# Kernel tuning notes

Measured on AMD Instinct MI355X. Metric: run time of the kernel, lower is better.

Reference implementation:

```python
import jax, jax.numpy as jnp
import numpy as np

# positions 0,1 = input tensor dims; positions 2,3 = output tensor dims (single entity type)

def _set_partitions(elems):
    if not elems:
        yield []
        return
    first, rest = elems[0], elems[1:]
    for p in _set_partitions(rest):
        for i in range(len(p)):
            yield p[:i] + [p[i] + [first]] + p[i + 1:]
    # note: generator above already covers merging; add singleton case

def _all_set_partitions(elems):
    if not elems:
        return [[]]
    first, rest = elems[0], elems[1:]
    out = []
    for p in _all_set_partitions(rest):
        for i in range(len(p)):
            out.append(p[:i] + [p[i] + [first]] + p[i + 1:])
        out.append([[first]] + p)
    return out

PARTITIONS = _all_set_partitions([0, 1, 2, 3])  # Bell(4) = 15 equivariant partitions


def _apply_partition(X, part, eye, ones):
    """Dense equivalent of diag -> pool -> broadcast -> undiag -> reindex for one partition.
    X: [b, c, n, n]. Returns [b, c, n, n]."""
    pos2blk = {p: bi for bi, blk in enumerate(part) for p in blk}
    blk_letter = {bi: 'defg'[bi] for bi in range(len(part))}
    # step 1: diag (repeated letters) + pool (letters dropped from output)
    in_sub = 'bc' + blk_letter[pos2blk[0]] + blk_letter[pos2blk[1]]
    keep = [bi for bi, blk in enumerate(part)
            if any(p < 2 for p in blk) and any(p >= 2 for p in blk)]
    z_sub = 'bc' + ''.join(blk_letter[bi] for bi in keep)
    Z = jnp.einsum(f'{in_sub}->{z_sub}', X)
    # step 2: broadcast + diag-embed into output positions via eye/ones factors
    out_letter = {2: 'p', 3: 'q'}
    operands, subs = [Z], [z_sub]
    for bi, blk in enumerate(part):
        outpos = [p for p in blk if p >= 2]
        if not outpos:
            continue
        if any(p < 2 for p in blk):  # block tied to a surviving input dim
            for p in outpos:
                operands.append(eye)
                subs.append(blk_letter[bi] + out_letter[p])
        else:  # pure broadcast block
            first = outpos[0]
            operands.append(ones)
            subs.append(out_letter[first])
            for p in outpos[1:]:
                operands.append(eye)
                subs.append(out_letter[first] + out_letter[p])
    return jnp.einsum(','.join(subs) + '->bcpq', *operands)


def setup_inputs() -> dict:
    key = jax.random.key(0)
    k1, k2 = jax.random.split(key)
    B, C_IN, C_OUT, N = 4, 96, 96, 256
    stdv = 0.1 / np.sqrt(C_IN)
    X_in = jax.random.normal(k1, (B, C_IN, N, N), dtype=jnp.float32)
    Y_in = jnp.zeros((B, C_IN, N, N), dtype=jnp.float32)  # only provides output shape
    weights = jax.random.uniform(k2, (15, C_IN, C_OUT), minval=-stdv, maxval=stdv, dtype=jnp.float32)
    bias = jnp.ones((1,), dtype=jnp.float32)
    return {'X_in': X_in, 'Y_in': Y_in, 'weights': weights, 'bias': bias}


def reference(X_in, Y_in, weights, bias):
    n = X_in.shape[-1]
    eye = jnp.eye(n, dtype=X_in.dtype)
    ones = jnp.ones((n,), dtype=X_in.dtype)
    Y = None
    for i, part in enumerate(PARTITIONS):
        Yp = _apply_partition(X_in, part, eye, ones)          # [b, c_in, n, n]
        Yp = jnp.einsum('bcpq,co->bopq', Yp, weights[i])       # channel linear
        Y = Yp if Y is None else Y + Yp
    return Y + bias[0]
```

## Files before the change

### kernel.cpp

```cpp
#include <hip/hip_runtime.h>
#include <hip/hip_bf16.h>

#define NN 256
#define CIN 96
#define COUT 96
#define BB 4
#define NBC (BB * CIN)
#define SEG (NBC * NN)

typedef __attribute__((ext_vector_type(8))) short short8;
typedef __attribute__((ext_vector_type(4))) float f32x4;

__device__ __forceinline__ float waveReduceSum(float v) {
    #pragma unroll
    for (int m = 32; m >= 1; m >>= 1) v += __shfl_xor(v, m, 64);
    return v;
}

__device__ __forceinline__ unsigned int packbf2(float lo, float hi) {
    __hip_bfloat162 h = __float22bfloat162_rn(make_float2(lo, hi));
    unsigned int u;
    __builtin_memcpy(&u, &h, 4);
    return u;
}

__device__ __forceinline__ short8 u4_to_s8(uint4 u) {
    short8 r;
    __builtin_memcpy(&r, &u, 16);
    return r;
}

__device__ __forceinline__ void lds_barrier() {
    __builtin_amdgcn_sched_barrier(0);
    asm volatile("s_waitcnt lgkmcnt(0)" ::: "memory");
    __builtin_amdgcn_s_barrier();
    __builtin_amdgcn_sched_barrier(0);
}

__global__ __launch_bounds__(256) void k_aux(const float* __restrict__ X,
                                             float* __restrict__ rows,
                                             float* __restrict__ diag,
                                             float* __restrict__ colsP,
                                             float* __restrict__ TSp) {
    const int blk = blockIdx.x;
    const int ch = blk & 3, bc = blk >> 2;
    const float* Xp = X + (size_t)bc * (NN * NN) + (size_t)ch * 64 * NN;
    const int tid = threadIdx.x;
    const int w = tid >> 6, lane = tid & 63;

    __shared__ float colPart[4][NN];
    __shared__ float sred[4];

    float4 csum = make_float4(0.f, 0.f, 0.f, 0.f);
    #pragma unroll
    for (int b2 = 0; b2 < 2; ++b2) {
        float4 v[8];
        #pragma unroll
        for (int j = 0; j < 8; ++j) {
            const int r = w * 16 + b2 * 8 + j;
            v[j] = *(const float4*)(Xp + (size_t)r * NN + lane * 4);
        }
        #pragma unroll
        for (int j = 0; j < 8; ++j) {
            csum.x += v[j].x; csum.y += v[j].y; csum.z += v[j].z; csum.w += v[j].w;
            float rs = waveReduceSum(v[j].x + v[j].y + v[j].z + v[j].w);
            if (lane == 0)
                rows[(size_t)bc * NN + ch * 64 + w * 16 + b2 * 8 + j] = rs;
        }
    }
    *(float4*)&colPart[w][lane * 4] = csum;

    if (w == 0) {
        float dv = Xp[(size_t)lane * NN + ch * 64 + lane];
        diag[(size_t)bc * NN + ch * 64 + lane] = dv;
        float t1 = waveReduceSum(dv);
        if (lane == 0) TSp[(ch * NBC + bc) * 2 + 0] = t1;
    }
    __syncthreads();

    float col = colPart[0][tid] + colPart[1][tid] + colPart[2][tid] + colPart[3][tid];
    colsP[(size_t)ch * SEG + (size_t)bc * NN + tid] = col;
    float s1 = waveReduceSum(col);
    if (lane == 0) sred[w] = s1;
    __syncthreads();
    if (tid == 0)
        TSp[(ch * NBC + bc) * 2 + 1] = sred[0] + sred[1] + sred[2] + sred[3];
}

__global__ __launch_bounds__(256) void k_sum(const float* __restrict__ colsP,
                                             const float* __restrict__ TSp,
                                             const float* __restrict__ W,
                                             float* __restrict__ cols,
                                             float* __restrict__ TSa,
                                             uint4* __restrict__ wpk) {
    const int blk = blockIdx.x;
    if (blk < NBC) {
        const int bc = blk;
        const int p = threadIdx.x;
        const size_t base = (size_t)bc * NN + p;
        cols[base] = colsP[0 * (size_t)SEG + base] + colsP[1 * (size_t)SEG + base]
                   + colsP[2 * (size_t)SEG + base] + colsP[3 * (size_t)SEG + base];
        if (p < 2)
            TSa[bc * 2 + p] = TSp[(0 * NBC + bc) * 2 + p] + TSp[(1 * NBC + bc) * 2 + p]
                            + TSp[(2 * NBC + bc) * 2 + p] + TSp[(3 * NBC + bc) * 2 + p];
    } else {
        const int e = (blk - NBC) * 256 + threadIdx.x;
        if (e < 2304) {
            const int lane = e & 63;
            const int pair = (e >> 6) & 1;
            const int sm = e >> 7;
            const int col = lane & 15, g = lane >> 4;
            const int s = sm / 6, m = sm - s * 6;
            const int o = m * 16 + col;
            const int cb = 32 * s + 8 * g;
            const float* wsrc = W + (pair ? 6 : 8) * CIN * COUT + (size_t)cb * COUT + o;
            uint4 v;
            v.x = packbf2(wsrc[0 * COUT], wsrc[1 * COUT]);
            v.y = packbf2(wsrc[2 * COUT], wsrc[3 * COUT]);
            v.z = packbf2(wsrc[4 * COUT], wsrc[5 * COUT]);
            v.w = packbf2(wsrc[6 * COUT], wsrc[7 * COUT]);
            wpk[e] = v;
        }
    }
}

__global__ __launch_bounds__(256) void k_pqg(const float* __restrict__ W,
                                             const float* __restrict__ rows,
                                             const float* __restrict__ cols,
                                             const float* __restrict__ diag,
                                             const float* __restrict__ TSa,
                                             const float* __restrict__ bias,
                                             float* __restrict__ Pw,
                                             float* __restrict__ Qw,
                                             float* __restrict__ Gw) {
    const int blk = blockIdx.x;
    const int bo = blk >> 1, ph = blk & 1;
    const int b = bo / COUT, o = bo % COUT;
    const int half = threadIdx.x >> 7;
    const int pl = threadIdx.x & 127;
    const int p = ph * 128 + pl;

    __shared__ float red[5][128];

    float P = 0.f, Q = 0.f, G = 0.f, s = 0.f, gs = 0.f;
    const int cbeg = half * 48, cend = cbeg + 48;
    for (int c = cbeg; c < cend; ++c) {
        const int bcq = b * CIN + c;
        const size_t base = (size_t)bcq * NN;
        float r  = rows[base + p];
        float cl = cols[base + p];
        float dg = diag[base + p];
        const float* wp = W + c * COUT + o;
        #define WI(i) wp[(i) * CIN * COUT]
        P += WI(12) * r + WI(7)  * cl + WI(5) * dg;
        Q += WI(13) * r + WI(10) * cl + WI(9) * dg;
        G += WI(3)  * r + WI(1)  * cl + WI(0) * dg;
        float Tv = TSa[bcq * 2 + 0];
        float Sv = TSa[bcq * 2 + 1];
        s  += WI(11) * Tv + WI(14) * Sv;
        gs += WI(2)  * Tv + WI(4)  * Sv;
        #undef WI
    }
    if (half == 1) {
        red[0][pl] = P; red[1][pl] = Q; red[2][pl] = G; red[3][pl] = s; red[4][pl] = gs;
    }
    __syncthreads();
    if (half == 0) {
        P += red[0][pl]; Q += red[1][pl]; G += red[2][pl]; s += red[3][pl]; gs += red[4][pl];
        const size_t ob = (size_t)bo * NN;
        Pw[ob + p] = P + s + bias[0];
        Qw[ob + p] = Q;
        Gw[ob + p] = G + gs;
    }
}

#define XAPLANE 260
#define XBPLANE 324

__global__ __launch_bounds__(512, 1) void k_main(const float* __restrict__ X,
                                                 const uint4* __restrict__ wpk,
                                                 const float* __restrict__ Pw,
                                                 const float* __restrict__ Qw,
                                                 const float* __restrict__ Gw,
                                                 float* __restrict__ Y) {
    __shared__ __align__(16) unsigned int XAs[16 * XAPLANE];
    __shared__ __align__(16) unsigned int XBs[16 * XBPLANE];
    __shared__ __align__(16) uint4 Wf[2304];

    const int orig = blockIdx.x + 16 * (blockIdx.y + 16 * blockIdx.z);
    const int work = (orig & 7) * 128 + (orig >> 3);
    const int tq = work & 15, tp = (work >> 4) & 15, b = work >> 8;

    const int tid = threadIdx.x;
    const int w = tid >> 6, lane = tid & 63;
    const int sp = lane >> 2, sq4 = (lane & 3) * 4;
    const int col = lane & 15, g = lane >> 4;

    const float* Xb  = X + (size_t)b * CIN * NN * NN;
    const float* G1  = Xb + (size_t)(tp * 16) * NN + tq * 16;
    const float* G2  = Xb + (size_t)(tq * 16) * NN + tp * 16;

    const int cw0 = w, cw1 = w + 8;

    float4 a00, a01, b00, b01, a10, a11, b10, b11;
    float4 c00, c01, d00, d01, c10, c11, d10, d11;

    #define LOADG_SET(C0, A00, A01, B00, B01, A10, A11, B10, B11) { \
        const size_t cb0 = (size_t)((C0) + 2 * cw0) * (NN * NN); \
        const size_t cb1 = (size_t)((C0) + 2 * cw1) * (NN * NN); \
        const float* pa0 = G1 + cb0 + sp * NN + sq4; \
        A00 = *(const float4*)pa0; \
        A01 = *(const float4*)(pa0 + NN * NN); \
        const float* pb0 = G2 + cb0 + sp * NN + sq4; \
        B00 = *(const float4*)pb0; \
        B01 = *(const float4*)(pb0 + NN * NN); \
        const float* pa1 = G1 + cb1 + sp * NN + sq4; \
        A10 = *(const float4*)pa1; \
        A11 = *(const float4*)(pa1 + NN * NN); \
        const float* pb1 = G2 + cb1 + sp * NN + sq4; \
        B10 = *(const float4*)pb1; \
        B11 = *(const float4*)(pb1 + NN * NN); }

    #define PACKSTORE(A00, A01, B00, B01, A10, A11, B10, B11) { \
        uint4 pk; \
        pk.x = packbf2(A00.x, A01.x); \
        pk.y = packbf2(A00.y, A01.y); \
        pk.z = packbf2(A00.z, A01.z); \
        pk.w = packbf2(A00.w, A01.w); \
        *(uint4*)&XAs[cw0 * XAPLANE + sp * 16 + sq4] = pk; \
        pk.x = packbf2(A10.x, A11.x); \
        pk.y = packbf2(A10.y, A11.y); \
        pk.z = packbf2(A10.z, A11.z); \
        pk.w = packbf2(A10.w, A11.w); \
        *(uint4*)&XAs[cw1 * XAPLANE + sp * 16 + sq4] = pk; \
        unsigned int* dB0 = &XBs[cw0 * XBPLANE + sp]; \
        dB0[(sq4 + 0) * 20] = packbf2(B00.x, B01.x); \
        dB0[(sq4 + 1) * 20] = packbf2(B00.y, B01.y); \
        dB0[(sq4 + 2) * 20] = packbf2(B00.z, B01.z); \
        dB0[(sq4 + 3) * 20] = packbf2(B00.w, B01.w); \
        unsigned int* dB1 = &XBs[cw1 * XBPLANE + sp]; \
        dB1[(sq4 + 0) * 20] = packbf2(B10.x, B11.x); \
        dB1[(sq4 + 1) * 20] = packbf2(B10.y, B11.y); \
        dB1[(sq4 + 2) * 20] = packbf2(B10.z, B11.z); \
        dB1[(sq4 + 3) * 20] = packbf2(B10.w, B11.w); }

    #define MSTEP(S, M) { \
        short8 w8f = u4_to_s8(wb[(M) * 128]); \
        short8 w6f = u4_to_s8(wb[(M) * 128 + 64]); \
        acc[M][0] = __builtin_amdgcn_mfma_f32_16x16x32_bf16(xd0, w8f, acc[M][0], 0, 0, 0); \
        acc[M][0] = __builtin_amdgcn_mfma_f32_16x16x32_bf16(xt0, w6f, acc[M][0], 0, 0, 0); \
        acc[M][1] = __builtin_amdgcn_mfma_f32_16x16x32_bf16(xd1, w8f, acc[M][1], 0, 0, 0); \
        acc[M][1] = __builtin_amdgcn_mfma_f32_16x16x32_bf16(xt1, w6f, acc[M][1], 0, 0, 0); }

    #define KCOMPUTE(S) { \
        const unsigned int* xab = &XAs[4 * g * XAPLANE + w * 16 + col]; \
        const unsigned int* xbb = &XBs[4 * g * XBPLANE + w * 20 + col]; \
        uint4 u; \
        u.x = xab[0]; u.y = xab[XAPLANE]; u.z = xab[2 * XAPLANE]; u.w = xab[3 * XAPLANE]; \
        short8 xd0 = u4_to_s8(u); \
        u.x = xab[128]; u.y = xab[XAPLANE + 128]; u.z = xab[2 * XAPLANE + 128]; u.w = xab[3 * XAPLANE + 128]; \
        short8 xd1 = u4_to_s8(u); \
        u.x = xbb[0]; u.y = xbb[XBPLANE]; u.z = xbb[2 * XBPLANE]; u.w = xbb[3 * XBPLANE]; \
        short8 xt0 = u4_to_s8(u); \
        u.x = xbb[160]; u.y = xbb[XBPLANE + 160]; u.z = xbb[2 * XBPLANE + 160]; u.w = xbb[3 * XBPLANE + 160]; \
        short8 xt1 = u4_to_s8(u); \
        const uint4* wb = &Wf[(S) * 768 + lane]; \
        MSTEP(S, 0) MSTEP(S, 1) MSTEP(S, 2) MSTEP(S, 3) MSTEP(S, 4) MSTEP(S, 5) }

    LOADG_SET(0,  a00, a01, b00, b01, a10, a11, b10, b11);
    LOADG_SET(32, c00, c01, d00, d01, c10, c11, d10, d11);
    for (int iw = tid; iw < 2304; iw += 512) Wf[iw] = wpk[iw];

    f32x4 acc[6][2];
    #pragma unroll
    for (int m = 0; m < 6; ++m) {
        acc[m][0] = f32x4{0.f, 0.f, 0.f, 0.f};
        acc[m][1] = f32x4{0.f, 0.f, 0.f, 0.f};
    }

    lds_barrier();
    PACKSTORE(a00, a01, b00, b01, a10, a11, b10, b11);
    lds_barrier();
    LOADG_SET(64, a00, a01, b00, b01, a10, a11, b10, b11);
    __builtin_amdgcn_sched_barrier(0);
    KCOMPUTE(0)

    lds_barrier();
    PACKSTORE(c00, c01, d00, d01, c10, c11, d10, d11);
    lds_barrier();
    KCOMPUTE(1)

    lds_barrier();
    PACKSTORE(a00, a01, b00, b01, a10, a11, b10, b11);
    lds_barrier();
    KCOMPUTE(2)

    #undef KCOMPUTE
    #undef MSTEP
    #undef PACKSTORE
    #undef LOADG_SET

    const int p0 = tp * 16 + w;
    const int q4 = tq * 16 + g * 4;
    const bool diagblk = (tp == tq);
    #pragma unroll
    for (int m = 0; m < 6; ++m) {
        const int o = m * 16 + col;
        const size_t ob = (size_t)(b * COUT + o) * NN;
        const float4 qf = *(const float4*)&Qw[ob + q4];
        #pragma unroll
        for (int rr = 0; rr < 2; ++rr) {
            const int p = p0 + rr * 8;
            const float pv = Pw[ob + p];
            float4 out;
            out.x = acc[m][rr][0] + pv + qf.x;
            out.y = acc[m][rr][1] + pv + qf.y;
            out.z = acc[m][rr][2] + pv + qf.z;
            out.w = acc[m][rr][3] + pv + qf.w;
            if (diagblk) {
                const float gv = Gw[ob + p];
                const int d = (p & 15) - g * 4;
                if (d == 0) out.x += gv;
                else if (d == 1) out.y += gv;
                else if (d == 2) out.z += gv;
                else if (d == 3) out.w += gv;
            }
            *(float4*)&Y[(ob + p) * NN + q4] = out;
        }
    }
}

extern "C" void kernel_launch(void* const* d_in, const int* in_sizes, int n_in,
                              void* d_out, int out_size, void* d_ws, size_t ws_size,
                              hipStream_t stream) {
    const float* X    = (const float*)d_in[0];
    const float* W    = (const float*)d_in[2];
    const float* bias = (const float*)d_in[3];
    float* Y = (float*)d_out;

    float* ws    = (float*)d_ws;
    float* rows  = ws;
    float* diag  = ws + (size_t)SEG;
    float* colsP = ws + 2 * (size_t)SEG;
    float* Pw    = ws + 6 * (size_t)SEG;
    float* Qw    = ws + 7 * (size_t)SEG;
    float* Gw    = ws + 8 * (size_t)SEG;
    float* TSp   = ws + 9 * (size_t)SEG;
    float* TSa   = ws + 9 * (size_t)SEG + 4096;
    float* cols  = ws + 10 * (size_t)SEG;
    uint4* wpk   = (uint4*)(ws + 11 * (size_t)SEG);

    k_aux<<<NBC * 4, 256, 0, stream>>>(X, rows, diag, colsP, TSp);
    k_sum<<<NBC + 9, 256, 0, stream>>>(colsP, TSp, W, cols, TSa, wpk);
    k_pqg<<<BB * COUT * 2, 256, 0, stream>>>(W, rows, cols, diag, TSa, bias, Pw, Qw, Gw);
    k_main<<<dim3(16, 16, BB), 512, 0, stream>>>(X, wpk, Pw, Qw, Gw, Y);
}
```

Before: 106.5 us.

## Process two adjacent output tiles per block with cross-tile load pipelining

```diff
diff --git a/kernel.cpp b/kernel.cpp
--- a/kernel.cpp
+++ b/kernel.cpp
@@ -28,13 +28,6 @@
     short8 r;
     __builtin_memcpy(&r, &u, 16);
     return r;
-}
-
-__device__ __forceinline__ void lds_barrier() {
-    __builtin_amdgcn_sched_barrier(0);
-    asm volatile("s_waitcnt lgkmcnt(0)" ::: "memory");
-    __builtin_amdgcn_s_barrier();
-    __builtin_amdgcn_sched_barrier(0);
 }
 
 __global__ __launch_bounds__(256) void k_aux(const float* __restrict__ X,
@@ -187,9 +180,10 @@
     __shared__ __align__(16) unsigned int XBs[16 * XBPLANE];
     __shared__ __align__(16) uint4 Wf[2304];
 
-    const int orig = blockIdx.x + 16 * (blockIdx.y + 16 * blockIdx.z);
-    const int work = (orig & 7) * 128 + (orig >> 3);
-    const int tq = work & 15, tp = (work >> 4) & 15, b = work >> 8;
+    const int orig = blockIdx.x;
+    const int kk = (orig & 7) * 64 + (orig >> 3);
+    const int W0 = kk << 1;
+    const int tq0 = W0 & 15, tp = (W0 >> 4) & 15, b = W0 >> 8;
 
     const int tid = threadIdx.x;
     const int w = tid >> 6, lane = tid & 63;
@@ -197,54 +191,56 @@
     const int col = lane & 15, g = lane >> 4;
 
     const float* Xb  = X + (size_t)b * CIN * NN * NN;
-    const float* G1  = Xb + (size_t)(tp * 16) * NN + tq * 16;
-    const float* G2  = Xb + (size_t)(tq * 16) * NN + tp * 16;
+    const float* G1a = Xb + (size_t)(tp * 16) * NN + tq0 * 16;
+    const float* G2a = Xb + (size_t)(tq0 * 16) * NN + tp * 16;
+    const float* G1b = G1a + 16;
+    const float* G2b = G2a + 16 * NN;
 
     const int cw0 = w, cw1 = w + 8;
 
-    float4 a00, a01, b00, b01, a10, a11, b10, b11;
-    float4 c00, c01, d00, d01, c10, c11, d10, d11;
-
-    #define LOADG_SET(C0, A00, A01, B00, B01, A10, A11, B10, B11) { \
+    float4 a00, a01, b00, b01;
+    float4 a10, a11, b10, b11;
+
+    #define LOADG(G1X, G2X, C0) { \
         const size_t cb0 = (size_t)((C0) + 2 * cw0) * (NN * NN); \
         const size_t cb1 = (size_t)((C0) + 2 * cw1) * (NN * NN); \
-        const float* pa0 = G1 + cb0 + sp * NN + sq4; \
-        A00 = *(const float4*)pa0; \
-        A01 = *(const float4*)(pa0 + NN * NN); \
-        const float* pb0 = G2 + cb0 + sp * NN + sq4; \
-        B00 = *(const float4*)pb0; \
-        B01 = *(const float4*)(pb0 + NN * NN); \
-        const float* pa1 = G1 + cb1 + sp * NN + sq4; \
-        A10 = *(const float4*)pa1; \
-        A11 = *(const float4*)(pa1 + NN * NN); \
-        const float* pb1 = G2 + cb1 + sp * NN + sq4; \
-        B10 = *(const float4*)pb1; \
-        B11 = *(const float4*)(pb1 + NN * NN); }
-
-    #define PACKSTORE(A00, A01, B00, B01, A10, A11, B10, B11) { \
+        const float* pa0 = (G1X) + cb0 + sp * NN + sq4; \
+        a00 = *(const float4*)pa0; \
+        a01 = *(const float4*)(pa0 + NN * NN); \
+        const float* pb0 = (G2X) + cb0 + sp * NN + sq4; \
+        b00 = *(const float4*)pb0; \
+        b01 = *(const float4*)(pb0 + NN * NN); \
+        const float* pa1 = (G1X) + cb1 + sp * NN + sq4; \
+        a10 = *(const float4*)pa1; \
+        a11 = *(const float4*)(pa1 + NN * NN); \
+        const float* pb1 = (G2X) + cb1 + sp * NN + sq4; \
+        b10 = *(const float4*)pb1; \
+        b11 = *(const float4*)(pb1 + NN * NN); }
+
+    #define PACKSTORE() { \
         uint4 pk; \
-        pk.x = packbf2(A00.x, A01.x); \
-        pk.y = packbf2(A00.y, A01.y); \
-        pk.z = packbf2(A00.z, A01.z); \
-        pk.w = packbf2(A00.w, A01.w); \
+        pk.x = packbf2(a00.x, a01.x); \
+        pk.y = packbf2(a00.y, a01.y); \
+        pk.z = packbf2(a00.z, a01.z); \
+        pk.w = packbf2(a00.w, a01.w); \
         *(uint4*)&XAs[cw0 * XAPLANE + sp * 16 + sq4] = pk; \
-        pk.x = packbf2(A10.x, A11.x); \
-        pk.y = packbf2(A10.y, A11.y); \
-        pk.z = packbf2(A10.z, A11.z); \
-        pk.w = packbf2(A10.w, A11.w); \
+        pk.x = packbf2(a10.x, a11.x); \
+        pk.y = packbf2(a10.y, a11.y); \
+        pk.z = packbf2(a10.z, a11.z); \
+        pk.w = packbf2(a10.w, a11.w); \
         *(uint4*)&XAs[cw1 * XAPLANE + sp * 16 + sq4] = pk; \
         unsigned int* dB0 = &XBs[cw0 * XBPLANE + sp]; \
-        dB0[(sq4 + 0) * 20] = packbf2(B00.x, B01.x); \
-        dB0[(sq4 + 1) * 20] = packbf2(B00.y, B01.y); \
-        dB0[(sq4 + 2) * 20] = packbf2(B00.z, B01.z); \
-        dB0[(sq4 + 3) * 20] = packbf2(B00.w, B01.w); \
+        dB0[(sq4 + 0) * 20] = packbf2(b00.x, b01.x); \
+        dB0[(sq4 + 1) * 20] = packbf2(b00.y, b01.y); \
+        dB0[(sq4 + 2) * 20] = packbf2(b00.z, b01.z); \
+        dB0[(sq4 + 3) * 20] = packbf2(b00.w, b01.w); \
         unsigned int* dB1 = &XBs[cw1 * XBPLANE + sp]; \
-        dB1[(sq4 + 0) * 20] = packbf2(B10.x, B11.x); \
-        dB1[(sq4 + 1) * 20] = packbf2(B10.y, B11.y); \
-        dB1[(sq4 + 2) * 20] = packbf2(B10.z, B11.z); \
-        dB1[(sq4 + 3) * 20] = packbf2(B10.w, B11.w); }
-
-    #define MSTEP(S, M) { \
+        dB1[(sq4 + 0) * 20] = packbf2(b10.x, b11.x); \
+        dB1[(sq4 + 1) * 20] = packbf2(b10.y, b11.y); \
+        dB1[(sq4 + 2) * 20] = packbf2(b10.z, b11.z); \
+        dB1[(sq4 + 3) * 20] = packbf2(b10.w, b11.w); }
+
+    #define MSTEP(M) { \
         short8 w8f = u4_to_s8(wb[(M) * 128]); \
         short8 w6f = u4_to_s8(wb[(M) * 128 + 64]); \
         acc[M][0] = __builtin_amdgcn_mfma_f32_16x16x32_bf16(xd0, w8f, acc[M][0], 0, 0, 0); \
@@ -265,10 +261,46 @@
         u.x = xbb[160]; u.y = xbb[XBPLANE + 160]; u.z = xbb[2 * XBPLANE + 160]; u.w = xbb[3 * XBPLANE + 160]; \
         short8 xt1 = u4_to_s8(u); \
         const uint4* wb = &Wf[(S) * 768 + lane]; \
-        MSTEP(S, 0) MSTEP(S, 1) MSTEP(S, 2) MSTEP(S, 3) MSTEP(S, 4) MSTEP(S, 5) }
-
-    LOADG_SET(0,  a00, a01, b00, b01, a10, a11, b10, b11);
-    LOADG_SET(32, c00, c01, d00, d01, c10, c11, d10, d11);
+        MSTEP(0) MSTEP(1) MSTEP(2) MSTEP(3) MSTEP(4) MSTEP(5) }
+
+    #define KSTEP(S, DOLOAD, G1X, G2X, C0) { \
+        __syncthreads(); \
+        PACKSTORE(); \
+        __syncthreads(); \
+        if (DOLOAD) { LOADG(G1X, G2X, C0); } \
+        KCOMPUTE(S) }
+
+    #define EPI_TILE(TQ) { \
+        const int p0 = tp * 16 + w; \
+        const int q4 = (TQ) * 16 + g * 4; \
+        const bool diagblk = (tp == (TQ)); \
+        _Pragma("unroll") \
+        for (int m = 0; m < 6; ++m) { \
+            const int o = m * 16 + col; \
+            const size_t ob = (size_t)(b * COUT + o) * NN; \
+            const float4 qf = *(const float4*)&Qw[ob + q4]; \
+            _Pragma("unroll") \
+            for (int rr = 0; rr < 2; ++rr) { \
+                const int p = p0 + rr * 8; \
+                const float pv = Pw[ob + p]; \
+                float4 out; \
+                out.x = acc[m][rr][0] + pv + qf.x; \
+                out.y = acc[m][rr][1] + pv + qf.y; \
+                out.z = acc[m][rr][2] + pv + qf.z; \
+                out.w = acc[m][rr][3] + pv + qf.w; \
+                if (diagblk) { \
+                    const float gv = Gw[ob + p]; \
+                    const int d = (p & 15) - g * 4; \
+                    if (d == 0) out.x += gv; \
+                    else if (d == 1) out.y += gv; \
+                    else if (d == 2) out.z += gv; \
+                    else if (d == 3) out.w += gv; \
+                } \
+                *(float4*)&Y[(ob + p) * NN + q4] = out; \
+            } \
+        } }
+
+    LOADG(G1a, G2a, 0);
     for (int iw = tid; iw < 2304; iw += 512) Wf[iw] = wpk[iw];
 
     f32x4 acc[6][2];
@@ -278,56 +310,28 @@
         acc[m][1] = f32x4{0.f, 0.f, 0.f, 0.f};
     }
 
-    lds_barrier();
-    PACKSTORE(a00, a01, b00, b01, a10, a11, b10, b11);
-    lds_barrier();
-    LOADG_SET(64, a00, a01, b00, b01, a10, a11, b10, b11);
-    __builtin_amdgcn_sched_barrier(0);
-    KCOMPUTE(0)
-
-    lds_barrier();
-    PACKSTORE(c00, c01, d00, d01, c10, c11, d10, d11);
-    lds_barrier();
-    KCOMPUTE(1)
-
-    lds_barrier();
-    PACKSTORE(a00, a01, b00, b01, a10, a11, b10, b11);
-    lds_barrier();
-    KCOMPUTE(2)
-
+    KSTEP(0, 1, G1a, G2a, 32)
+    KSTEP(1, 1, G1a, G2a, 64)
+    KSTEP(2, 1, G1b, G2b, 0)
+    EPI_TILE(tq0)
+
+    #pragma unroll
+    for (int m = 0; m < 6; ++m) {
+        acc[m][0] = f32x4{0.f, 0.f, 0.f, 0.f};
+        acc[m][1] = f32x4{0.f, 0.f, 0.f, 0.f};
+    }
+
+    KSTEP(0, 1, G1b, G2b, 32)
+    KSTEP(1, 1, G1b, G2b, 64)
+    KSTEP(2, 0, G1b, G2b, 0)
+    EPI_TILE(tq0 + 1)
+
+    #undef EPI_TILE
+    #undef KSTEP
     #undef KCOMPUTE
     #undef MSTEP
     #undef PACKSTORE
-    #undef LOADG_SET
-
-    const int p0 = tp * 16 + w;
-    const int q4 = tq * 16 + g * 4;
-    const bool diagblk = (tp == tq);
-    #pragma unroll
-    for (int m = 0; m < 6; ++m) {
-        const int o = m * 16 + col;
-        const size_t ob = (size_t)(b * COUT + o) * NN;
-        const float4 qf = *(const float4*)&Qw[ob + q4];
-        #pragma unroll
-        for (int rr = 0; rr < 2; ++rr) {
-            const int p = p0 + rr * 8;
-            const float pv = Pw[ob + p];
-            float4 out;
-            out.x = acc[m][rr][0] + pv + qf.x;
-            out.y = acc[m][rr][1] + pv + qf.y;
-            out.z = acc[m][rr][2] + pv + qf.z;
-            out.w = acc[m][rr][3] + pv + qf.w;
-            if (diagblk) {
-                const float gv = Gw[ob + p];
-                const int d = (p & 15) - g * 4;
-                if (d == 0) out.x += gv;
-                else if (d == 1) out.y += gv;
-                else if (d == 2) out.z += gv;
-                else if (d == 3) out.w += gv;
-            }
-            *(float4*)&Y[(ob + p) * NN + q4] = out;
-        }
-    }
+    #undef LOADG
 }
 
 extern "C" void kernel_launch(void* const* d_in, const int* in_sizes, int n_in,
@@ -353,5 +357,5 @@
     k_aux<<<NBC * 4, 256, 0, stream>>>(X, rows, diag, colsP, TSp);
     k_sum<<<NBC + 9, 256, 0, stream>>>(colsP, TSp, W, cols, TSa, wpk);
     k_pqg<<<BB * COUT * 2, 256, 0, stream>>>(W, rows, cols, diag, TSa, bias, Pw, Qw, Gw);
-    k_main<<<dim3(16, 16, BB), 512, 0, stream>>>(X, wpk, Pw, Qw, Gw, Y);
-}
+    k_main<<<512, 512, 0, stream>>>(X, wpk, Pw, Qw, Gw, Y);
+}
```

Result: slower. 121.5 us (+14.1%).
